# Optimization experiments

Measured on AMD Instinct MI355X. Metric: run time of the kernel, lower is better.

Reference implementation:

```python
import jax, jax.numpy as jnp
import numpy as np


def reference(x, edge_index, edge_attr, W, b):
    """PyG GCNConv: out = D^{-1/2} (A + I) D^{-1/2} X W + b.

    x: [N, Din] node features
    edge_index: [2, E] int (row=source, col=target)
    edge_attr: [E] edge weights
    W: [Din, Dout], b: [Dout]
    """
    N = x.shape[0]
    # add self-loops with weight 1 (PyG fill_value=1.0)
    loop = jnp.arange(N, dtype=edge_index.dtype)
    row = jnp.concatenate([edge_index[0], loop])
    col = jnp.concatenate([edge_index[1], loop])
    w = jnp.concatenate([edge_attr, jnp.ones((N,), dtype=edge_attr.dtype)])

    # symmetric normalization: norm_e = d[row]^-1/2 * w_e * d[col]^-1/2
    deg = jax.ops.segment_sum(w, col, num_segments=N)
    dis = jnp.where(deg > 0, jax.lax.rsqrt(jnp.where(deg > 0, deg, 1.0)), 0.0)
    norm = dis[row] * w * dis[col]

    # linear projection first (Din == Dout, cheaper either way), then
    # gather-scale-scatter aggregation at targets
    h = x @ W                                   # [N, Dout]
    msg = h[row] * norm[:, None]                # [E+N, Dout]
    out = jax.ops.segment_sum(msg, col, num_segments=N)  # [N, Dout]
    return out + b


def setup_inputs() -> dict:
    key = jax.random.key(0)
    k1, k2, k3, k4 = jax.random.split(key, 4)
    N, E, Din, Dout = 100000, 1600000, 128, 128
    x = jax.random.normal(k1, (N, Din), dtype=jnp.float32)
    edge_index = jax.random.randint(k2, (2, E), 0, N, dtype=jnp.int64)
    edge_attr = jax.random.uniform(k3, (E,), dtype=jnp.float32)
    # Glorot init like PyG Linear default
    W = jax.random.normal(k4, (Din, Dout), dtype=jnp.float32) * (1.0 / np.sqrt(Din))
    b = jnp.zeros((Dout,), dtype=jnp.float32)
    return {"x": x, "edge_index": edge_index, "edge_attr": edge_attr, "W": W, "b": b}
```

## Files before the change

kernel.cpp:

```cpp
#include <hip/hip_runtime.h>


#define ELEMS_PER_SCAN_BLOCK 4096
#define SCAN_SHIFT 12
#define CHUNK 2048

typedef __attribute__((ext_vector_type(8))) short short8;
typedef __attribute__((ext_vector_type(4))) float f32x4;

__device__ inline unsigned short f2bf(float f) {
    unsigned u = __float_as_uint(f);
    u += 0x7fffu + ((u >> 16) & 1u);
    return (unsigned short)(u >> 16);
}
__device__ inline float bf_lo(unsigned u) { return __uint_as_float(u << 16); }
__device__ inline float bf_hi(unsigned u) { return __uint_as_float(u & 0xffff0000u); }

union SmemU {
    struct { short Xs[64][136]; short Ws[128][136]; } g;
    struct { int lcnt[1024]; int gadj[1024]; int2 stage[CHUNK]; int sdst[CHUNK];
             int wsum[4]; int woff[4]; } p;
    struct { int2 sbuf[3072]; int cnt128[128]; float degf[128]; int cur128[128];
             int wtot[2]; } f;
};

__global__ __launch_bounds__(256) void k_hist(const int* __restrict__ col,
                                              const float* __restrict__ W,
                                              int* __restrict__ histg,
                                              unsigned short* __restrict__ Wtg,
                                              int E, int NC, int NBLK) {
    __shared__ int lh[1024];
    int t = threadIdx.x, blk = blockIdx.x;
    if (blk < 64) {
        int n = blk * 2 + (t >> 7);
        int k = t & 127;
        Wtg[n * 128 + k] = f2bf(W[k * 128 + n]);
    }
    for (int i = t; i < 1024; i += 256) lh[i] = 0;
    __syncthreads();
    int base = blk * CHUNK;
    #pragma unroll
    for (int i = 0; i < CHUNK / 256; ++i) {
        int e = base + i * 256 + t;
        if (e < E) atomicAdd(&lh[col[e] >> 7], 1);
    }
    __syncthreads();
    for (int b = t; b < NC; b += 256) histg[b * NBLK + blk] = lh[b];
}

__device__ inline int wave_incl_scan(int x, int lane) {
    #pragma unroll
    for (int d = 1; d < 64; d <<= 1) {
        int y = __shfl_up(x, d, 64);
        if (lane >= d) x += y;
    }
    return x;
}

__global__ void k_scan1(const int* __restrict__ in, int* __restrict__ out,
                        int* __restrict__ bsum, int M) {
    __shared__ int wsum[4];
    __shared__ int woff[4];
    int t = threadIdx.x, lane = t & 63, wid = t >> 6;
    int base = blockIdx.x * ELEMS_PER_SCAN_BLOCK + t * 16;
    int v[16];
    #pragma unroll
    for (int i = 0; i < 16; ++i) v[i] = (base + i < M) ? in[base + i] : 0;
    int run = 0;
    #pragma unroll
    for (int i = 0; i < 16; ++i) { int x = v[i]; v[i] = run; run += x; }
    int incl = wave_incl_scan(run, lane);
    int excl = incl - run;
    if (lane == 63) wsum[wid] = incl;
    __syncthreads();
    if (t == 0) {
        int r = 0;
        #pragma unroll
        for (int w = 0; w < 4; ++w) { int s = wsum[w]; woff[w] = r; r += s; }
        bsum[blockIdx.x] = r;
    }
    __syncthreads();
    int off = woff[wid] + excl;
    #pragma unroll
    for (int i = 0; i < 16; ++i)
        if (base + i < M) out[base + i] = v[i] + off;
}

__global__ void k_scan2(const int* __restrict__ bsum, int* __restrict__ boff, int NB) {
    __shared__ int wsum[4];
    __shared__ int woff[4];
    int t = threadIdx.x, lane = t & 63, wid = t >> 6;
    int x = (t < NB) ? bsum[t] : 0;
    int incl = wave_incl_scan(x, lane);
    int excl = incl - x;
    if (lane == 63) wsum[wid] = incl;
    __syncthreads();
    if (t == 0) {
        int r = 0;
        #pragma unroll
        for (int w = 0; w < 4; ++w) { int s = wsum[w]; woff[w] = r; r += s; }
    }
    __syncthreads();
    if (t < NB) boff[t] = woff[wid] + excl;
}

__device__ __forceinline__ void gemm_body(SmemU& sm, const float* __restrict__ x,
                                          const unsigned short* __restrict__ Wtg,
                                          unsigned short* __restrict__ h,
                                          int row0, int N, int t) {
    int lane = t & 63, wid = t >> 6;
    {
        int r = t >> 2;
        int kseg = (t & 3) * 32;
        int gr = row0 + r;
        const float4* src = (const float4*)(x + (size_t)gr * 128 + kseg);
        #pragma unroll
        for (int i = 0; i < 4; ++i) {
            float4 v0 = make_float4(0.f, 0.f, 0.f, 0.f), v1 = v0;
            if (gr < N) { v0 = src[2 * i]; v1 = src[2 * i + 1]; }
            short8 p;
            p[0] = (short)f2bf(v0.x); p[1] = (short)f2bf(v0.y);
            p[2] = (short)f2bf(v0.z); p[3] = (short)f2bf(v0.w);
            p[4] = (short)f2bf(v1.x); p[5] = (short)f2bf(v1.y);
            p[6] = (short)f2bf(v1.z); p[7] = (short)f2bf(v1.w);
            *(short8*)&sm.g.Xs[r][kseg + 8 * i] = p;
        }
    }
    {
        int n = t >> 1;
        int seg = (t & 1) * 64;
        const short* wsrc = (const short*)Wtg + n * 128 + seg;
        #pragma unroll
        for (int i = 0; i < 8; ++i)
            *(short8*)&sm.g.Ws[n][seg + 8 * i] = *(const short8*)(wsrc + 8 * i);
    }
    __syncthreads();

    int q = lane >> 4;
    int m = lane & 15;
    f32x4 acc[8];
    #pragma unroll
    for (int tde = 0; tde < 8; ++tde) acc[tde] = (f32x4){0.f, 0.f, 0.f, 0.f};
    #pragma unroll
    for (int kc = 0; kc < 128; kc += 32) {
        short8 af = *(const short8*)&sm.g.Xs[wid * 16 + m][kc + q * 8];
        #pragma unroll
        for (int tde = 0; tde < 8; ++tde) {
            short8 bf = *(const short8*)&sm.g.Ws[tde * 16 + m][kc + q * 8];
            acc[tde] = __builtin_amdgcn_mfma_f32_16x16x32_bf16(af, bf, acc[tde], 0, 0, 0);
        }
    }
    #pragma unroll
    for (int r = 0; r < 4; ++r) {
        int grow = row0 + wid * 16 + q * 4 + r;
        if (grow < N) {
            #pragma unroll
            for (int tde = 0; tde < 8; ++tde)
                h[(size_t)grow * 128 + tde * 16 + m] = f2bf(acc[tde][r]);
        }
    }
}

__global__ __launch_bounds__(256) void k_pg(const int* __restrict__ row,
                                            const int* __restrict__ col,
                                            const float* __restrict__ wgt,
                                            const int* __restrict__ histg,
                                            const int* __restrict__ boff,
                                            int2* __restrict__ srw,
                                            const float* __restrict__ x,
                                            const unsigned short* __restrict__ Wtg,
                                            unsigned short* __restrict__ h,
                                            int E, int N, int NC, int NBLK) {
    __shared__ SmemU sm;
    int t = threadIdx.x;
    if ((int)blockIdx.x >= NBLK) {
        gemm_body(sm, x, Wtg, h, ((int)blockIdx.x - NBLK) * 64, N, t);
        return;
    }
    int blk = blockIdx.x;
    int lane = t & 63, wid = t >> 6;
    int base = blk * CHUNK;
    int nE = min(CHUNK, E - base);
    for (int b = t; b < 1024; b += 256) sm.p.lcnt[b] = 0;
    __syncthreads();
    #pragma unroll
    for (int i = 0; i < CHUNK / 256; ++i) {
        int e = base + i * 256 + t;
        if (e < E) atomicAdd(&sm.p.lcnt[col[e] >> 7], 1);
    }
    __syncthreads();
    int c4[4];
    int sum = 0;
    #pragma unroll
    for (int i = 0; i < 4; ++i) { int v = sm.p.lcnt[t * 4 + i]; c4[i] = sum; sum += v; }
    int incl = wave_incl_scan(sum, lane);
    int excl = incl - sum;
    if (lane == 63) sm.p.wsum[wid] = incl;
    __syncthreads();
    if (t == 0) {
        int r = 0;
        #pragma unroll
        for (int w = 0; w < 4; ++w) { int s = sm.p.wsum[w]; sm.p.woff[w] = r; r += s; }
    }
    __syncthreads();
    int tb = sm.p.woff[wid] + excl;
    __syncthreads();
    #pragma unroll
    for (int i = 0; i < 4; ++i) {
        int idx = t * 4 + i;
        int b0 = tb + c4[i];
        int gb = 0;
        if (idx < NC) {
            int g = idx * NBLK + blk;
            gb = histg[g] + boff[g >> SCAN_SHIFT];
        }
        sm.p.gadj[idx] = gb - b0;
        sm.p.lcnt[idx] = b0;
    }
    __syncthreads();
    #pragma unroll
    for (int i = 0; i < CHUNK / 256; ++i) {
        int e = base + i * 256 + t;
        if (e < E) {
            int c = col[e];
            int slot = atomicAdd(&sm.p.lcnt[c >> 7], 1);
            sm.p.stage[slot] = make_int2(((c & 127) << 17) | row[e], __float_as_int(wgt[e]));
            sm.p.sdst[slot] = sm.p.gadj[c >> 7] + slot;
        }
    }
    __syncthreads();
    for (int s_ = t; s_ < nE; s_ += 256) {
        srw[sm.p.sdst[s_]] = sm.p.stage[s_];
    }
}

__global__ __launch_bounds__(256) void k_fg(const int* __restrict__ histg,
                                            const int* __restrict__ boff,
                                            const int2* __restrict__ srw,
                                            int* __restrict__ rowptr,
                                            float* __restrict__ dis,
                                            int2* __restrict__ spack,
                                            const float* __restrict__ x,
                                            const unsigned short* __restrict__ Wtg,
                                            unsigned short* __restrict__ h,
                                            int E, int N, int NC, int NBLK, int GB1) {
    __shared__ SmemU sm;
    int t = threadIdx.x;
    if ((int)blockIdx.x >= NC) {
        gemm_body(sm, x, Wtg, h, (GB1 + (int)blockIdx.x - NC) * 64, N, t);
        return;
    }
    int b = blockIdx.x;
    int nb = b << 7;
    int g0 = b * NBLK;
    int start = histg[g0] + boff[g0 >> SCAN_SHIFT];
    int end;
    if (b == NC - 1) end = E;
    else {
        int g1 = (b + 1) * NBLK;
        end = histg[g1] + boff[g1 >> SCAN_SHIFT];
    }
    int cnt = end - start;
    int NL = min(cnt, 3072);
    if (t < 128) { sm.f.cnt128[t] = 0; sm.f.degf[t] = 1.0f; }
    __syncthreads();
    for (int j = t; j < cnt; j += 256) {
        int2 s = srw[start + j];
        if (j < NL) sm.f.sbuf[j] = s;
        int c = s.x >> 17;
        atomicAdd(&sm.f.cnt128[c], 1);
        atomicAdd(&sm.f.degf[c], __int_as_float(s.y));
    }
    __syncthreads();
    int v = 0, incl = 0;
    if (t < 128) {
        v = sm.f.cnt128[t];
        incl = wave_incl_scan(v, t & 63);
        if ((t & 63) == 63) sm.f.wtot[t >> 6] = incl;
    }
    __syncthreads();
    if (t < 128) {
        int excl = incl - v + ((t >= 64) ? sm.f.wtot[0] : 0);
        int p = start + excl;
        sm.f.cur128[t] = p;
        int n = nb + t;
        if (n < N) {
            rowptr[n] = p;
            dis[n] = rsqrtf(sm.f.degf[t]);
        }
    }
    if (t == 0 && b == NC - 1) rowptr[N] = E;
    __syncthreads();
    for (int j = t; j < cnt; j += 256) {
        int2 s = (j < NL) ? sm.f.sbuf[j] : srw[start + j];
        int c = s.x >> 17;
        int pos = atomicAdd(&sm.f.cur128[c], 1);
        spack[pos] = make_int2(s.x & 0x1FFFF, s.y);
    }
}

__global__ __launch_bounds__(256) void k_gather(const unsigned int* __restrict__ hb,
                                                const float* __restrict__ dis,
                                                const int* __restrict__ rowptr,
                                                const long* __restrict__ spackl,
                                                const float* __restrict__ bias,
                                                float* __restrict__ out, int N) {
    int gid = blockIdx.x * blockDim.x + threadIdx.x;
    int node = gid >> 6;
    int lane = gid & 63;
    if (node >= N) return;
    node = __builtin_amdgcn_readfirstlane(node);

    float dn = dis[node];
    unsigned u = hb[(size_t)node * 64 + lane];
    float2 acc;
    acc.x = dn * bf_lo(u);
    acc.y = dn * bf_hi(u);

    int jb = rowptr[node], je = rowptr[node + 1];
    int j = jb;
    long q0, q1, q2, q3, q4, q5, q6, q7;
    if (j + 8 <= je) {
        q0 = __builtin_nontemporal_load(spackl + j);
        q1 = __builtin_nontemporal_load(spackl + j + 1);
        q2 = __builtin_nontemporal_load(spackl + j + 2);
        q3 = __builtin_nontemporal_load(spackl + j + 3);
        q4 = __builtin_nontemporal_load(spackl + j + 4);
        q5 = __builtin_nontemporal_load(spackl + j + 5);
        q6 = __builtin_nontemporal_load(spackl + j + 6);
        q7 = __builtin_nontemporal_load(spackl + j + 7);
    }
    for (; j + 8 <= je; j += 8) {
        int r0 = __builtin_amdgcn_readfirstlane((int)q0);
        int r1 = __builtin_amdgcn_readfirstlane((int)q1);
        int r2 = __builtin_amdgcn_readfirstlane((int)q2);
        int r3 = __builtin_amdgcn_readfirstlane((int)q3);
        int r4 = __builtin_amdgcn_readfirstlane((int)q4);
        int r5 = __builtin_amdgcn_readfirstlane((int)q5);
        int r6 = __builtin_amdgcn_readfirstlane((int)q6);
        int r7 = __builtin_amdgcn_readfirstlane((int)q7);
        unsigned u0 = hb[(size_t)r0 * 64 + lane];
        unsigned u1 = hb[(size_t)r1 * 64 + lane];
        unsigned u2 = hb[(size_t)r2 * 64 + lane];
        unsigned u3 = hb[(size_t)r3 * 64 + lane];
        unsigned u4 = hb[(size_t)r4 * 64 + lane];
        unsigned u5 = hb[(size_t)r5 * 64 + lane];
        unsigned u6 = hb[(size_t)r6 * 64 + lane];
        unsigned u7 = hb[(size_t)r7 * 64 + lane];
        int jn = (j + 16 <= je) ? j + 8 : j;
        long n0 = __builtin_nontemporal_load(spackl + jn);
        long n1 = __builtin_nontemporal_load(spackl + jn + 1);
        long n2 = __builtin_nontemporal_load(spackl + jn + 2);
        long n3 = __builtin_nontemporal_load(spackl + jn + 3);
        long n4 = __builtin_nontemporal_load(spackl + jn + 4);
        long n5 = __builtin_nontemporal_load(spackl + jn + 5);
        long n6 = __builtin_nontemporal_load(spackl + jn + 6);
        long n7 = __builtin_nontemporal_load(spackl + jn + 7);
        float a0 = dis[r0] * __uint_as_float((unsigned)((unsigned long)q0 >> 32));
        float a1 = dis[r1] * __uint_as_float((unsigned)((unsigned long)q1 >> 32));
        float a2 = dis[r2] * __uint_as_float((unsigned)((unsigned long)q2 >> 32));
        float a3 = dis[r3] * __uint_as_float((unsigned)((unsigned long)q3 >> 32));
        float a4 = dis[r4] * __uint_as_float((unsigned)((unsigned long)q4 >> 32));
        float a5 = dis[r5] * __uint_as_float((unsigned)((unsigned long)q5 >> 32));
        float a6 = dis[r6] * __uint_as_float((unsigned)((unsigned long)q6 >> 32));
        float a7 = dis[r7] * __uint_as_float((unsigned)((unsigned long)q7 >> 32));
        acc.x = fmaf(a0, bf_lo(u0), acc.x); acc.y = fmaf(a0, bf_hi(u0), acc.y);
        acc.x = fmaf(a1, bf_lo(u1), acc.x); acc.y = fmaf(a1, bf_hi(u1), acc.y);
        acc.x = fmaf(a2, bf_lo(u2), acc.x); acc.y = fmaf(a2, bf_hi(u2), acc.y);
        acc.x = fmaf(a3, bf_lo(u3), acc.x); acc.y = fmaf(a3, bf_hi(u3), acc.y);
        acc.x = fmaf(a4, bf_lo(u4), acc.x); acc.y = fmaf(a4, bf_hi(u4), acc.y);
        acc.x = fmaf(a5, bf_lo(u5), acc.x); acc.y = fmaf(a5, bf_hi(u5), acc.y);
        acc.x = fmaf(a6, bf_lo(u6), acc.x); acc.y = fmaf(a6, bf_hi(u6), acc.y);
        acc.x = fmaf(a7, bf_lo(u7), acc.x); acc.y = fmaf(a7, bf_hi(u7), acc.y);
        q0 = n0; q1 = n1; q2 = n2; q3 = n3; q4 = n4; q5 = n5; q6 = n6; q7 = n7;
    }
    for (; j < je; ++j) {
        long q = __builtin_nontemporal_load(spackl + j);
        int r = __builtin_amdgcn_readfirstlane((int)q);
        unsigned uu = hb[(size_t)r * 64 + lane];
        float a = dis[r] * __uint_as_float((unsigned)((unsigned long)q >> 32));
        acc.x = fmaf(a, bf_lo(uu), acc.x);
        acc.y = fmaf(a, bf_hi(uu), acc.y);
    }

    int c0 = lane * 2;
    float2 bv = *(const float2*)(bias + c0);
    float2 o;
    o.x = bv.x + dn * acc.x;
    o.y = bv.y + dn * acc.y;
    union { float2 f; double d; } cvt;
    cvt.f = o;
    __builtin_nontemporal_store(cvt.d, (double*)(out + (size_t)node * 128 + c0));
}

extern "C" void kernel_launch(void* const* d_in, const int* in_sizes, int n_in,
                              void* d_out, int out_size, void* d_ws, size_t ws_size,
                              hipStream_t stream) {
    const float* x     = (const float*)d_in[0];
    const int*   eidx  = (const int*)d_in[1];
    const float* eattr = (const float*)d_in[2];
    const float* W     = (const float*)d_in[3];
    const float* bias  = (const float*)d_in[4];
    int N = in_sizes[0] / 128;
    int E = in_sizes[2];
    const int* row = eidx;
    const int* col = eidx + E;

    int NC = (N + 127) >> 7;
    int NBLK = (E + CHUNK - 1) / CHUNK;

    char* p = (char*)d_ws;
    auto carve = [&](size_t bytes) {
        char* q = p;
        p += (bytes + 255) & ~(size_t)255;
        return q;
    };
    unsigned short* h   = (unsigned short*)carve((size_t)N * 128 * sizeof(unsigned short));
    unsigned short* Wtg = (unsigned short*)carve(128 * 128 * sizeof(unsigned short));
    float* dis    = (float*)carve((size_t)N * sizeof(float));
    int*   rowptr = (int*)carve((size_t)(N + 1) * sizeof(int));
    int*   histg  = (int*)carve((size_t)NC * NBLK * sizeof(int));
    int2*  srw    = (int2*)carve((size_t)E * sizeof(int2));
    int2*  spack  = (int2*)carve((size_t)E * sizeof(int2));
    int*   bsum   = (int*)carve(256 * sizeof(int));
    int*   boff   = (int*)carve(256 * sizeof(int));

    int M = NC * NBLK;
    int NBs = (M + ELEMS_PER_SCAN_BLOCK - 1) / ELEMS_PER_SCAN_BLOCK;

    int GB  = (N + 63) / 64;
    int GB1 = GB / 2;
    int GB2 = GB - GB1;

    k_hist<<<NBLK, 256, 0, stream>>>(col, W, histg, Wtg, E, NC, NBLK);
    k_scan1<<<NBs, 256, 0, stream>>>(histg, histg, bsum, M);
    k_scan2<<<1, 256, 0, stream>>>(bsum, boff, NBs);
    k_pg<<<NBLK + GB1, 256, 0, stream>>>(row, col, eattr, histg, boff, srw,
                                         x, Wtg, h, E, N, NC, NBLK);
    k_fg<<<NC + GB2, 256, 0, stream>>>(histg, boff, srw, rowptr, dis, spack,
                                       x, Wtg, h, E, N, NC, NBLK, GB1);
    {
        size_t threads = (size_t)N * 64;
        int blocks = (int)((threads + 255) / 256);
        k_gather<<<blocks, 256, 0, stream>>>((const unsigned int*)h, dis, rowptr,
                                             (const long*)spack, bias, (float*)d_out, N);
    }
}
```

Before: 261.0 us.

## Replace two-pass bucket sort CSR build with per-node atomic counting sort

Drops the 128-node-bucket histogram and the two-stage partition (k_pg staging plus k_fg finalize). It now builds CSR with global per-node atomic degree counts, a scan over N, and a single atomic scatter pass that also accumulates weighted degree. The inverse-sqrt degree is computed on the fly in the gather instead of being stored as a dis array. This cuts kernel launches and the intermediate srw buffer, but adds a memset and many global atomics with random scatter writes. The order of edges within each node's list becomes nondeterministic.

```diff
diff --git a/kernel.cpp b/kernel.cpp
--- a/kernel.cpp
+++ b/kernel.cpp
@@ -3,7 +3,8 @@
 
 #define ELEMS_PER_SCAN_BLOCK 4096
 #define SCAN_SHIFT 12
-#define CHUNK 2048
+#define CHUNK_D 4096
+#define CHUNK_P 2048
 
 typedef __attribute__((ext_vector_type(8))) short short8;
 typedef __attribute__((ext_vector_type(4))) float f32x4;
@@ -16,36 +17,23 @@
 __device__ inline float bf_lo(unsigned u) { return __uint_as_float(u << 16); }
 __device__ inline float bf_hi(unsigned u) { return __uint_as_float(u & 0xffff0000u); }
 
-union SmemU {
-    struct { short Xs[64][136]; short Ws[128][136]; } g;
-    struct { int lcnt[1024]; int gadj[1024]; int2 stage[CHUNK]; int sdst[CHUNK];
-             int wsum[4]; int woff[4]; } p;
-    struct { int2 sbuf[3072]; int cnt128[128]; float degf[128]; int cur128[128];
-             int wtot[2]; } f;
-};
-
-__global__ __launch_bounds__(256) void k_hist(const int* __restrict__ col,
-                                              const float* __restrict__ W,
-                                              int* __restrict__ histg,
-                                              unsigned short* __restrict__ Wtg,
-                                              int E, int NC, int NBLK) {
-    __shared__ int lh[1024];
+__global__ __launch_bounds__(256) void k_deg(const int* __restrict__ col,
+                                             const float* __restrict__ W,
+                                             int* __restrict__ cnt,
+                                             unsigned short* __restrict__ Wtg,
+                                             int E) {
     int t = threadIdx.x, blk = blockIdx.x;
     if (blk < 64) {
         int n = blk * 2 + (t >> 7);
         int k = t & 127;
         Wtg[n * 128 + k] = f2bf(W[k * 128 + n]);
     }
-    for (int i = t; i < 1024; i += 256) lh[i] = 0;
-    __syncthreads();
-    int base = blk * CHUNK;
-    #pragma unroll
-    for (int i = 0; i < CHUNK / 256; ++i) {
+    int base = blk * CHUNK_D;
+    #pragma unroll
+    for (int i = 0; i < CHUNK_D / 256; ++i) {
         int e = base + i * 256 + t;
-        if (e < E) atomicAdd(&lh[col[e] >> 7], 1);
-    }
-    __syncthreads();
-    for (int b = t; b < NC; b += 256) histg[b * NBLK + blk] = lh[b];
+        if (e < E) atomicAdd(&cnt[col[e]], 1);
+    }
 }
 
 __device__ inline int wave_incl_scan(int x, int lane) {
@@ -86,7 +74,8 @@
         if (base + i < M) out[base + i] = v[i] + off;
 }
 
-__global__ void k_scan2(const int* __restrict__ bsum, int* __restrict__ boff, int NB) {
+__global__ void k_scan2(const int* __restrict__ bsum, int* __restrict__ boff,
+                        int* __restrict__ rowptr, int N, int E, int NB) {
     __shared__ int wsum[4];
     __shared__ int woff[4];
     int t = threadIdx.x, lane = t & 63, wid = t >> 6;
@@ -101,10 +90,16 @@
         for (int w = 0; w < 4; ++w) { int s = wsum[w]; woff[w] = r; r += s; }
     }
     __syncthreads();
-    if (t < NB) boff[t] = woff[wid] + excl;
-}
-
-__device__ __forceinline__ void gemm_body(SmemU& sm, const float* __restrict__ x,
+    if (t < NB) {
+        int b = woff[wid] + excl;
+        boff[t] = b;
+        if (t == (N >> SCAN_SHIFT)) rowptr[N] = E - b;
+    }
+}
+
+struct GSmem { short Xs[64][136]; short Ws[128][136]; };
+
+__device__ __forceinline__ void gemm_body(GSmem& sm, const float* __restrict__ x,
                                           const unsigned short* __restrict__ Wtg,
                                           unsigned short* __restrict__ h,
                                           int row0, int N, int t) {
@@ -123,7 +118,7 @@
             p[2] = (short)f2bf(v0.z); p[3] = (short)f2bf(v0.w);
             p[4] = (short)f2bf(v1.x); p[5] = (short)f2bf(v1.y);
             p[6] = (short)f2bf(v1.z); p[7] = (short)f2bf(v1.w);
-            *(short8*)&sm.g.Xs[r][kseg + 8 * i] = p;
+            *(short8*)&sm.Xs[r][kseg + 8 * i] = p;
         }
     }
     {
@@ -132,7 +127,7 @@
         const short* wsrc = (const short*)Wtg + n * 128 + seg;
         #pragma unroll
         for (int i = 0; i < 8; ++i)
-            *(short8*)&sm.g.Ws[n][seg + 8 * i] = *(const short8*)(wsrc + 8 * i);
+            *(short8*)&sm.Ws[n][seg + 8 * i] = *(const short8*)(wsrc + 8 * i);
     }
     __syncthreads();
 
@@ -143,10 +138,10 @@
     for (int tde = 0; tde < 8; ++tde) acc[tde] = (f32x4){0.f, 0.f, 0.f, 0.f};
     #pragma unroll
     for (int kc = 0; kc < 128; kc += 32) {
-        short8 af = *(const short8*)&sm.g.Xs[wid * 16 + m][kc + q * 8];
+        short8 af = *(const short8*)&sm.Xs[wid * 16 + m][kc + q * 8];
         #pragma unroll
         for (int tde = 0; tde < 8; ++tde) {
-            short8 bf = *(const short8*)&sm.g.Ws[tde * 16 + m][kc + q * 8];
+            short8 bf = *(const short8*)&sm.Ws[tde * 16 + m][kc + q * 8];
             acc[tde] = __builtin_amdgcn_mfma_f32_16x16x32_bf16(af, bf, acc[tde], 0, 0, 0);
         }
     }
@@ -164,144 +159,40 @@
 __global__ __launch_bounds__(256) void k_pg(const int* __restrict__ row,
                                             const int* __restrict__ col,
                                             const float* __restrict__ wgt,
-                                            const int* __restrict__ histg,
+                                            const int* __restrict__ rowptr,
                                             const int* __restrict__ boff,
-                                            int2* __restrict__ srw,
-                                            const float* __restrict__ x,
-                                            const unsigned short* __restrict__ Wtg,
-                                            unsigned short* __restrict__ h,
-                                            int E, int N, int NC, int NBLK) {
-    __shared__ SmemU sm;
-    int t = threadIdx.x;
-    if ((int)blockIdx.x >= NBLK) {
-        gemm_body(sm, x, Wtg, h, ((int)blockIdx.x - NBLK) * 64, N, t);
-        return;
-    }
-    int blk = blockIdx.x;
-    int lane = t & 63, wid = t >> 6;
-    int base = blk * CHUNK;
-    int nE = min(CHUNK, E - base);
-    for (int b = t; b < 1024; b += 256) sm.p.lcnt[b] = 0;
-    __syncthreads();
-    #pragma unroll
-    for (int i = 0; i < CHUNK / 256; ++i) {
-        int e = base + i * 256 + t;
-        if (e < E) atomicAdd(&sm.p.lcnt[col[e] >> 7], 1);
-    }
-    __syncthreads();
-    int c4[4];
-    int sum = 0;
-    #pragma unroll
-    for (int i = 0; i < 4; ++i) { int v = sm.p.lcnt[t * 4 + i]; c4[i] = sum; sum += v; }
-    int incl = wave_incl_scan(sum, lane);
-    int excl = incl - sum;
-    if (lane == 63) sm.p.wsum[wid] = incl;
-    __syncthreads();
-    if (t == 0) {
-        int r = 0;
-        #pragma unroll
-        for (int w = 0; w < 4; ++w) { int s = sm.p.wsum[w]; sm.p.woff[w] = r; r += s; }
-    }
-    __syncthreads();
-    int tb = sm.p.woff[wid] + excl;
-    __syncthreads();
-    #pragma unroll
-    for (int i = 0; i < 4; ++i) {
-        int idx = t * 4 + i;
-        int b0 = tb + c4[i];
-        int gb = 0;
-        if (idx < NC) {
-            int g = idx * NBLK + blk;
-            gb = histg[g] + boff[g >> SCAN_SHIFT];
-        }
-        sm.p.gadj[idx] = gb - b0;
-        sm.p.lcnt[idx] = b0;
-    }
-    __syncthreads();
-    #pragma unroll
-    for (int i = 0; i < CHUNK / 256; ++i) {
-        int e = base + i * 256 + t;
-        if (e < E) {
-            int c = col[e];
-            int slot = atomicAdd(&sm.p.lcnt[c >> 7], 1);
-            sm.p.stage[slot] = make_int2(((c & 127) << 17) | row[e], __float_as_int(wgt[e]));
-            sm.p.sdst[slot] = sm.p.gadj[c >> 7] + slot;
-        }
-    }
-    __syncthreads();
-    for (int s_ = t; s_ < nE; s_ += 256) {
-        srw[sm.p.sdst[s_]] = sm.p.stage[s_];
-    }
-}
-
-__global__ __launch_bounds__(256) void k_fg(const int* __restrict__ histg,
-                                            const int* __restrict__ boff,
-                                            const int2* __restrict__ srw,
-                                            int* __restrict__ rowptr,
-                                            float* __restrict__ dis,
+                                            int* __restrict__ cnt,
+                                            float* __restrict__ degf,
                                             int2* __restrict__ spack,
                                             const float* __restrict__ x,
                                             const unsigned short* __restrict__ Wtg,
                                             unsigned short* __restrict__ h,
-                                            int E, int N, int NC, int NBLK, int GB1) {
-    __shared__ SmemU sm;
+                                            int E, int N, int NBLKP) {
+    __shared__ GSmem sm;
     int t = threadIdx.x;
-    if ((int)blockIdx.x >= NC) {
-        gemm_body(sm, x, Wtg, h, (GB1 + (int)blockIdx.x - NC) * 64, N, t);
+    if ((int)blockIdx.x >= NBLKP) {
+        gemm_body(sm, x, Wtg, h, ((int)blockIdx.x - NBLKP) * 64, N, t);
         return;
     }
-    int b = blockIdx.x;
-    int nb = b << 7;
-    int g0 = b * NBLK;
-    int start = histg[g0] + boff[g0 >> SCAN_SHIFT];
-    int end;
-    if (b == NC - 1) end = E;
-    else {
-        int g1 = (b + 1) * NBLK;
-        end = histg[g1] + boff[g1 >> SCAN_SHIFT];
-    }
-    int cnt = end - start;
-    int NL = min(cnt, 3072);
-    if (t < 128) { sm.f.cnt128[t] = 0; sm.f.degf[t] = 1.0f; }
-    __syncthreads();
-    for (int j = t; j < cnt; j += 256) {
-        int2 s = srw[start + j];
-        if (j < NL) sm.f.sbuf[j] = s;
-        int c = s.x >> 17;
-        atomicAdd(&sm.f.cnt128[c], 1);
-        atomicAdd(&sm.f.degf[c], __int_as_float(s.y));
-    }
-    __syncthreads();
-    int v = 0, incl = 0;
-    if (t < 128) {
-        v = sm.f.cnt128[t];
-        incl = wave_incl_scan(v, t & 63);
-        if ((t & 63) == 63) sm.f.wtot[t >> 6] = incl;
-    }
-    __syncthreads();
-    if (t < 128) {
-        int excl = incl - v + ((t >= 64) ? sm.f.wtot[0] : 0);
-        int p = start + excl;
-        sm.f.cur128[t] = p;
-        int n = nb + t;
-        if (n < N) {
-            rowptr[n] = p;
-            dis[n] = rsqrtf(sm.f.degf[t]);
+    int base = (int)blockIdx.x * CHUNK_P;
+    #pragma unroll
+    for (int i = 0; i < CHUNK_P / 256; ++i) {
+        int e = base + i * 256 + t;
+        if (e < E) {
+            int c = col[e];
+            float w = wgt[e];
+            atomicAdd(&degf[c], w);
+            int old = atomicSub(&cnt[c], 1);
+            int pos = rowptr[c] + boff[c >> SCAN_SHIFT] + old - 1;
+            spack[pos] = make_int2(row[e], __float_as_int(w));
         }
     }
-    if (t == 0 && b == NC - 1) rowptr[N] = E;
-    __syncthreads();
-    for (int j = t; j < cnt; j += 256) {
-        int2 s = (j < NL) ? sm.f.sbuf[j] : srw[start + j];
-        int c = s.x >> 17;
-        int pos = atomicAdd(&sm.f.cur128[c], 1);
-        spack[pos] = make_int2(s.x & 0x1FFFF, s.y);
-    }
 }
 
 __global__ __launch_bounds__(256) void k_gather(const unsigned int* __restrict__ hb,
-                                                const float* __restrict__ dis,
+                                                const float* __restrict__ degf,
                                                 const int* __restrict__ rowptr,
+                                                const int* __restrict__ boff,
                                                 const long* __restrict__ spackl,
                                                 const float* __restrict__ bias,
                                                 float* __restrict__ out, int N) {
@@ -311,13 +202,14 @@
     if (node >= N) return;
     node = __builtin_amdgcn_readfirstlane(node);
 
-    float dn = dis[node];
+    float dn = __frsqrt_rn(degf[node] + 1.0f);
     unsigned u = hb[(size_t)node * 64 + lane];
     float2 acc;
     acc.x = dn * bf_lo(u);
     acc.y = dn * bf_hi(u);
 
-    int jb = rowptr[node], je = rowptr[node + 1];
+    int jb = rowptr[node] + boff[node >> SCAN_SHIFT];
+    int je = rowptr[node + 1] + boff[(node + 1) >> SCAN_SHIFT];
     int j = jb;
     long q0, q1, q2, q3, q4, q5, q6, q7;
     if (j + 8 <= je) {
@@ -356,14 +248,14 @@
         long n5 = __builtin_nontemporal_load(spackl + jn + 5);
         long n6 = __builtin_nontemporal_load(spackl + jn + 6);
         long n7 = __builtin_nontemporal_load(spackl + jn + 7);
-        float a0 = dis[r0] * __uint_as_float((unsigned)((unsigned long)q0 >> 32));
-        float a1 = dis[r1] * __uint_as_float((unsigned)((unsigned long)q1 >> 32));
-        float a2 = dis[r2] * __uint_as_float((unsigned)((unsigned long)q2 >> 32));
-        float a3 = dis[r3] * __uint_as_float((unsigned)((unsigned long)q3 >> 32));
-        float a4 = dis[r4] * __uint_as_float((unsigned)((unsigned long)q4 >> 32));
-        float a5 = dis[r5] * __uint_as_float((unsigned)((unsigned long)q5 >> 32));
-        float a6 = dis[r6] * __uint_as_float((unsigned)((unsigned long)q6 >> 32));
-        float a7 = dis[r7] * __uint_as_float((unsigned)((unsigned long)q7 >> 32));
+        float a0 = __frsqrt_rn(degf[r0] + 1.0f) * __uint_as_float((unsigned)((unsigned long)q0 >> 32));
+        float a1 = __frsqrt_rn(degf[r1] + 1.0f) * __uint_as_float((unsigned)((unsigned long)q1 >> 32));
+        float a2 = __frsqrt_rn(degf[r2] + 1.0f) * __uint_as_float((unsigned)((unsigned long)q2 >> 32));
+        float a3 = __frsqrt_rn(degf[r3] + 1.0f) * __uint_as_float((unsigned)((unsigned long)q3 >> 32));
+        float a4 = __frsqrt_rn(degf[r4] + 1.0f) * __uint_as_float((unsigned)((unsigned long)q4 >> 32));
+        float a5 = __frsqrt_rn(degf[r5] + 1.0f) * __uint_as_float((unsigned)((unsigned long)q5 >> 32));
+        float a6 = __frsqrt_rn(degf[r6] + 1.0f) * __uint_as_float((unsigned)((unsigned long)q6 >> 32));
+        float a7 = __frsqrt_rn(degf[r7] + 1.0f) * __uint_as_float((unsigned)((unsigned long)q7 >> 32));
         acc.x = fmaf(a0, bf_lo(u0), acc.x); acc.y = fmaf(a0, bf_hi(u0), acc.y);
         acc.x = fmaf(a1, bf_lo(u1), acc.x); acc.y = fmaf(a1, bf_hi(u1), acc.y);
         acc.x = fmaf(a2, bf_lo(u2), acc.x); acc.y = fmaf(a2, bf_hi(u2), acc.y);
@@ -378,7 +270,7 @@
         long q = __builtin_nontemporal_load(spackl + j);
         int r = __builtin_amdgcn_readfirstlane((int)q);
         unsigned uu = hb[(size_t)r * 64 + lane];
-        float a = dis[r] * __uint_as_float((unsigned)((unsigned long)q >> 32));
+        float a = __frsqrt_rn(degf[r] + 1.0f) * __uint_as_float((unsigned)((unsigned long)q >> 32));
         acc.x = fmaf(a, bf_lo(uu), acc.x);
         acc.y = fmaf(a, bf_hi(uu), acc.y);
     }
@@ -406,9 +298,6 @@
     const int* row = eidx;
     const int* col = eidx + E;
 
-    int NC = (N + 127) >> 7;
-    int NBLK = (E + CHUNK - 1) / CHUNK;
-
     char* p = (char*)d_ws;
     auto carve = [&](size_t bytes) {
         char* q = p;
@@ -417,32 +306,29 @@
     };
     unsigned short* h   = (unsigned short*)carve((size_t)N * 128 * sizeof(unsigned short));
     unsigned short* Wtg = (unsigned short*)carve(128 * 128 * sizeof(unsigned short));
-    float* dis    = (float*)carve((size_t)N * sizeof(float));
+    char* zbase = carve((size_t)2 * N * sizeof(int));
+    int*   cnt  = (int*)zbase;
+    float* degf = (float*)(zbase + (size_t)N * sizeof(int));
     int*   rowptr = (int*)carve((size_t)(N + 1) * sizeof(int));
-    int*   histg  = (int*)carve((size_t)NC * NBLK * sizeof(int));
-    int2*  srw    = (int2*)carve((size_t)E * sizeof(int2));
     int2*  spack  = (int2*)carve((size_t)E * sizeof(int2));
     int*   bsum   = (int*)carve(256 * sizeof(int));
     int*   boff   = (int*)carve(256 * sizeof(int));
 
-    int M = NC * NBLK;
-    int NBs = (M + ELEMS_PER_SCAN_BLOCK - 1) / ELEMS_PER_SCAN_BLOCK;
-
+    int NBLKD = (E + CHUNK_D - 1) / CHUNK_D;
+    int NBLKP = (E + CHUNK_P - 1) / CHUNK_P;
+    int NBs = (N + ELEMS_PER_SCAN_BLOCK - 1) / ELEMS_PER_SCAN_BLOCK;
     int GB  = (N + 63) / 64;
-    int GB1 = GB / 2;
-    int GB2 = GB - GB1;
-
-    k_hist<<<NBLK, 256, 0, stream>>>(col, W, histg, Wtg, E, NC, NBLK);
-    k_scan1<<<NBs, 256, 0, stream>>>(histg, histg, bsum, M);
-    k_scan2<<<1, 256, 0, stream>>>(bsum, boff, NBs);
-    k_pg<<<NBLK + GB1, 256, 0, stream>>>(row, col, eattr, histg, boff, srw,
-                                         x, Wtg, h, E, N, NC, NBLK);
-    k_fg<<<NC + GB2, 256, 0, stream>>>(histg, boff, srw, rowptr, dis, spack,
-                                       x, Wtg, h, E, N, NC, NBLK, GB1);
+
+    hipMemsetAsync(zbase, 0, (size_t)2 * N * sizeof(int), stream);
+    k_deg<<<NBLKD, 256, 0, stream>>>(col, W, cnt, Wtg, E);
+    k_scan1<<<NBs, 256, 0, stream>>>(cnt, rowptr, bsum, N);
+    k_scan2<<<1, 256, 0, stream>>>(bsum, boff, rowptr, N, E, NBs);
+    k_pg<<<NBLKP + GB, 256, 0, stream>>>(row, col, eattr, rowptr, boff, cnt, degf,
+                                         spack, x, Wtg, h, E, N, NBLKP);
     {
         size_t threads = (size_t)N * 64;
         int blocks = (int)((threads + 255) / 256);
-        k_gather<<<blocks, 256, 0, stream>>>((const unsigned int*)h, dis, rowptr,
+        k_gather<<<blocks, 256, 0, stream>>>((const unsigned int*)h, degf, rowptr, boff,
                                              (const long*)spack, bias, (float*)d_out, N);
     }
 }
```

Result: slower. 418.4 us (+60.3%).

## Shrink shared memory per kernel and move all GEMM blocks into partition kernel

Applied to the files above, without the earlier changes.

Splits the shared-memory union so each kernel declares only the storage it uses. The GEMM now stages K in two 64-wide halves, which shrinks its LDS tile, and the partition-side arrays are capped at 800 coarse buckets. All GEMM blocks now run alongside the partition kernel, so the fine-grouping kernel no longer carries GEMM work and has a small LDS footprint. The aim is higher occupancy and better overlap; the costs are an extra barrier pair in the GEMM and the risk that NC exceeds the hardcoded 800-bucket limit.

```diff
diff --git a/kernel.cpp b/kernel.cpp
--- a/kernel.cpp
+++ b/kernel.cpp
@@ -4,6 +4,7 @@
 #define ELEMS_PER_SCAN_BLOCK 4096
 #define SCAN_SHIFT 12
 #define CHUNK 2048
+#define NCMAX 800
 
 typedef __attribute__((ext_vector_type(8))) short short8;
 typedef __attribute__((ext_vector_type(4))) float f32x4;
@@ -15,14 +16,6 @@
 }
 __device__ inline float bf_lo(unsigned u) { return __uint_as_float(u << 16); }
 __device__ inline float bf_hi(unsigned u) { return __uint_as_float(u & 0xffff0000u); }
-
-union SmemU {
-    struct { short Xs[64][136]; short Ws[128][136]; } g;
-    struct { int lcnt[1024]; int gadj[1024]; int2 stage[CHUNK]; int sdst[CHUNK];
-             int wsum[4]; int woff[4]; } p;
-    struct { int2 sbuf[3072]; int cnt128[128]; float degf[128]; int cur128[128];
-             int wtot[2]; } f;
-};
 
 __global__ __launch_bounds__(256) void k_hist(const int* __restrict__ col,
                                               const float* __restrict__ W,
@@ -104,51 +97,59 @@
     if (t < NB) boff[t] = woff[wid] + excl;
 }
 
-__device__ __forceinline__ void gemm_body(SmemU& sm, const float* __restrict__ x,
+struct GSmem { short Xs[64][72]; short Ws[128][72]; };
+
+__device__ __forceinline__ void gemm_body(GSmem& sm, const float* __restrict__ x,
                                           const unsigned short* __restrict__ Wtg,
                                           unsigned short* __restrict__ h,
                                           int row0, int N, int t) {
     int lane = t & 63, wid = t >> 6;
-    {
-        int r = t >> 2;
-        int kseg = (t & 3) * 32;
-        int gr = row0 + r;
-        const float4* src = (const float4*)(x + (size_t)gr * 128 + kseg);
-        #pragma unroll
-        for (int i = 0; i < 4; ++i) {
-            float4 v0 = make_float4(0.f, 0.f, 0.f, 0.f), v1 = v0;
-            if (gr < N) { v0 = src[2 * i]; v1 = src[2 * i + 1]; }
-            short8 p;
-            p[0] = (short)f2bf(v0.x); p[1] = (short)f2bf(v0.y);
-            p[2] = (short)f2bf(v0.z); p[3] = (short)f2bf(v0.w);
-            p[4] = (short)f2bf(v1.x); p[5] = (short)f2bf(v1.y);
-            p[6] = (short)f2bf(v1.z); p[7] = (short)f2bf(v1.w);
-            *(short8*)&sm.g.Xs[r][kseg + 8 * i] = p;
-        }
-    }
-    {
-        int n = t >> 1;
-        int seg = (t & 1) * 64;
-        const short* wsrc = (const short*)Wtg + n * 128 + seg;
-        #pragma unroll
-        for (int i = 0; i < 8; ++i)
-            *(short8*)&sm.g.Ws[n][seg + 8 * i] = *(const short8*)(wsrc + 8 * i);
-    }
-    __syncthreads();
-
     int q = lane >> 4;
     int m = lane & 15;
     f32x4 acc[8];
     #pragma unroll
     for (int tde = 0; tde < 8; ++tde) acc[tde] = (f32x4){0.f, 0.f, 0.f, 0.f};
-    #pragma unroll
-    for (int kc = 0; kc < 128; kc += 32) {
-        short8 af = *(const short8*)&sm.g.Xs[wid * 16 + m][kc + q * 8];
+
+    #pragma unroll
+    for (int kh = 0; kh < 2; ++kh) {
+        {
+            int r = t >> 2;
+            int kf = (t & 3) * 16;
+            int gr = row0 + r;
+            const float4* src = (const float4*)(x + (size_t)gr * 128 + kh * 64 + kf);
+            float4 a0 = make_float4(0.f, 0.f, 0.f, 0.f), a1 = a0, a2 = a0, a3 = a0;
+            if (gr < N) { a0 = src[0]; a1 = src[1]; a2 = src[2]; a3 = src[3]; }
+            short8 p0, p1;
+            p0[0] = (short)f2bf(a0.x); p0[1] = (short)f2bf(a0.y);
+            p0[2] = (short)f2bf(a0.z); p0[3] = (short)f2bf(a0.w);
+            p0[4] = (short)f2bf(a1.x); p0[5] = (short)f2bf(a1.y);
+            p0[6] = (short)f2bf(a1.z); p0[7] = (short)f2bf(a1.w);
+            p1[0] = (short)f2bf(a2.x); p1[1] = (short)f2bf(a2.y);
+            p1[2] = (short)f2bf(a2.z); p1[3] = (short)f2bf(a2.w);
+            p1[4] = (short)f2bf(a3.x); p1[5] = (short)f2bf(a3.y);
+            p1[6] = (short)f2bf(a3.z); p1[7] = (short)f2bf(a3.w);
+            *(short8*)&sm.Xs[r][kf]     = p0;
+            *(short8*)&sm.Xs[r][kf + 8] = p1;
+        }
+        {
+            int n = t >> 1;
+            int off = (t & 1) * 32;
+            const short* wsrc = (const short*)Wtg + n * 128 + kh * 64 + off;
+            #pragma unroll
+            for (int i = 0; i < 4; ++i)
+                *(short8*)&sm.Ws[n][off + 8 * i] = *(const short8*)(wsrc + 8 * i);
+        }
+        __syncthreads();
         #pragma unroll
-        for (int tde = 0; tde < 8; ++tde) {
-            short8 bf = *(const short8*)&sm.g.Ws[tde * 16 + m][kc + q * 8];
-            acc[tde] = __builtin_amdgcn_mfma_f32_16x16x32_bf16(af, bf, acc[tde], 0, 0, 0);
-        }
+        for (int kc = 0; kc < 64; kc += 32) {
+            short8 af = *(const short8*)&sm.Xs[wid * 16 + m][kc + q * 8];
+            #pragma unroll
+            for (int tde = 0; tde < 8; ++tde) {
+                short8 bf = *(const short8*)&sm.Ws[tde * 16 + m][kc + q * 8];
+                acc[tde] = __builtin_amdgcn_mfma_f32_16x16x32_bf16(af, bf, acc[tde], 0, 0, 0);
+            }
+        }
+        __syncthreads();
     }
     #pragma unroll
     for (int r = 0; r < 4; ++r) {
@@ -171,17 +172,21 @@
                                             const unsigned short* __restrict__ Wtg,
                                             unsigned short* __restrict__ h,
                                             int E, int N, int NC, int NBLK) {
-    __shared__ SmemU sm;
+    __shared__ union {
+        struct { int lcnt[NCMAX]; int gadj[NCMAX]; int2 stage[CHUNK]; int sdst[CHUNK];
+                 int wsum[4]; int woff[4]; } p;
+        GSmem g;
+    } sm;
     int t = threadIdx.x;
     if ((int)blockIdx.x >= NBLK) {
-        gemm_body(sm, x, Wtg, h, ((int)blockIdx.x - NBLK) * 64, N, t);
+        gemm_body(sm.g, x, Wtg, h, ((int)blockIdx.x - NBLK) * 64, N, t);
         return;
     }
     int blk = blockIdx.x;
     int lane = t & 63, wid = t >> 6;
     int base = blk * CHUNK;
     int nE = min(CHUNK, E - base);
-    for (int b = t; b < 1024; b += 256) sm.p.lcnt[b] = 0;
+    for (int b = t; b < NCMAX; b += 256) sm.p.lcnt[b] = 0;
     __syncthreads();
     #pragma unroll
     for (int i = 0; i < CHUNK / 256; ++i) {
@@ -192,7 +197,11 @@
     int c4[4];
     int sum = 0;
     #pragma unroll
-    for (int i = 0; i < 4; ++i) { int v = sm.p.lcnt[t * 4 + i]; c4[i] = sum; sum += v; }
+    for (int i = 0; i < 4; ++i) {
+        int idx = t * 4 + i;
+        int v = (idx < NCMAX) ? sm.p.lcnt[idx] : 0;
+        c4[i] = sum; sum += v;
+    }
     int incl = wave_incl_scan(sum, lane);
     int excl = incl - sum;
     if (lane == 63) sm.p.wsum[wid] = incl;
@@ -208,14 +217,16 @@
     #pragma unroll
     for (int i = 0; i < 4; ++i) {
         int idx = t * 4 + i;
-        int b0 = tb + c4[i];
-        int gb = 0;
-        if (idx < NC) {
-            int g = idx * NBLK + blk;
-            gb = histg[g] + boff[g >> SCAN_SHIFT];
-        }
-        sm.p.gadj[idx] = gb - b0;
-        sm.p.lcnt[idx] = b0;
+        if (idx < NCMAX) {
+            int b0 = tb + c4[i];
+            int gb = 0;
+            if (idx < NC) {
+                int g = idx * NBLK + blk;
+                gb = histg[g] + boff[g >> SCAN_SHIFT];
+            }
+            sm.p.gadj[idx] = gb - b0;
+            sm.p.lcnt[idx] = b0;
+        }
     }
     __syncthreads();
     #pragma unroll
@@ -234,23 +245,16 @@
     }
 }
 
-__global__ __launch_bounds__(256) void k_fg(const int* __restrict__ histg,
-                                            const int* __restrict__ boff,
-                                            const int2* __restrict__ srw,
-                                            int* __restrict__ rowptr,
-                                            float* __restrict__ dis,
-                                            int2* __restrict__ spack,
-                                            const float* __restrict__ x,
-                                            const unsigned short* __restrict__ Wtg,
-                                            unsigned short* __restrict__ h,
-                                            int E, int N, int NC, int NBLK, int GB1) {
-    __shared__ SmemU sm;
-    int t = threadIdx.x;
-    if ((int)blockIdx.x >= NC) {
-        gemm_body(sm, x, Wtg, h, (GB1 + (int)blockIdx.x - NC) * 64, N, t);
-        return;
-    }
-    int b = blockIdx.x;
+__global__ __launch_bounds__(256) void k_fine(const int* __restrict__ histg,
+                                              const int* __restrict__ boff,
+                                              const int2* __restrict__ srw,
+                                              int* __restrict__ rowptr,
+                                              float* __restrict__ dis,
+                                              int2* __restrict__ spack,
+                                              int E, int N, int NC, int NBLK) {
+    __shared__ struct { int2 sbuf[3072]; int cnt128[128]; float degf[128];
+                        int cur128[128]; int wtot[2]; } sf;
+    int t = threadIdx.x, b = blockIdx.x;
     int nb = b << 7;
     int g0 = b * NBLK;
     int start = histg[g0] + boff[g0 >> SCAN_SHIFT];
@@ -262,39 +266,39 @@
     }
     int cnt = end - start;
     int NL = min(cnt, 3072);
-    if (t < 128) { sm.f.cnt128[t] = 0; sm.f.degf[t] = 1.0f; }
+    if (t < 128) { sf.cnt128[t] = 0; sf.degf[t] = 1.0f; }
     __syncthreads();
     for (int j = t; j < cnt; j += 256) {
         int2 s = srw[start + j];
-        if (j < NL) sm.f.sbuf[j] = s;
+        if (j < NL) sf.sbuf[j] = s;
         int c = s.x >> 17;
-        atomicAdd(&sm.f.cnt128[c], 1);
-        atomicAdd(&sm.f.degf[c], __int_as_float(s.y));
+        atomicAdd(&sf.cnt128[c], 1);
+        atomicAdd(&sf.degf[c], __int_as_float(s.y));
     }
     __syncthreads();
     int v = 0, incl = 0;
     if (t < 128) {
-        v = sm.f.cnt128[t];
+        v = sf.cnt128[t];
         incl = wave_incl_scan(v, t & 63);
-        if ((t & 63) == 63) sm.f.wtot[t >> 6] = incl;
+        if ((t & 63) == 63) sf.wtot[t >> 6] = incl;
     }
     __syncthreads();
     if (t < 128) {
-        int excl = incl - v + ((t >= 64) ? sm.f.wtot[0] : 0);
+        int excl = incl - v + ((t >= 64) ? sf.wtot[0] : 0);
         int p = start + excl;
-        sm.f.cur128[t] = p;
+        sf.cur128[t] = p;
         int n = nb + t;
         if (n < N) {
             rowptr[n] = p;
-            dis[n] = rsqrtf(sm.f.degf[t]);
+            dis[n] = rsqrtf(sf.degf[t]);
         }
     }
     if (t == 0 && b == NC - 1) rowptr[N] = E;
     __syncthreads();
     for (int j = t; j < cnt; j += 256) {
-        int2 s = (j < NL) ? sm.f.sbuf[j] : srw[start + j];
+        int2 s = (j < NL) ? sf.sbuf[j] : srw[start + j];
         int c = s.x >> 17;
-        int pos = atomicAdd(&sm.f.cur128[c], 1);
+        int pos = atomicAdd(&sf.cur128[c], 1);
         spack[pos] = make_int2(s.x & 0x1FFFF, s.y);
     }
 }
@@ -427,18 +431,14 @@
 
     int M = NC * NBLK;
     int NBs = (M + ELEMS_PER_SCAN_BLOCK - 1) / ELEMS_PER_SCAN_BLOCK;
-
-    int GB  = (N + 63) / 64;
-    int GB1 = GB / 2;
-    int GB2 = GB - GB1;
+    int GB = (N + 63) / 64;
 
     k_hist<<<NBLK, 256, 0, stream>>>(col, W, histg, Wtg, E, NC, NBLK);
     k_scan1<<<NBs, 256, 0, stream>>>(histg, histg, bsum, M);
     k_scan2<<<1, 256, 0, stream>>>(bsum, boff, NBs);
-    k_pg<<<NBLK + GB1, 256, 0, stream>>>(row, col, eattr, histg, boff, srw,
-                                         x, Wtg, h, E, N, NC, NBLK);
-    k_fg<<<NC + GB2, 256, 0, stream>>>(histg, boff, srw, rowptr, dis, spack,
-                                       x, Wtg, h, E, N, NC, NBLK, GB1);
+    k_pg<<<NBLK + GB, 256, 0, stream>>>(row, col, eattr, histg, boff, srw,
+                                        x, Wtg, h, E, N, NC, NBLK);
+    k_fine<<<NC, 256, 0, stream>>>(histg, boff, srw, rowptr, dis, spack, E, N, NC, NBLK);
     {
         size_t threads = (size_t)N * 64;
         int blocks = (int)((threads + 255) / 256);
```

After: 248.5 us. 1.05x faster.
